# Optimization experiments

Hardware: AMD Instinct MI355X
Metric: run time of the kernel (lower is better)

The kernel has to match this reference:

```python
import jax, jax.numpy as jnp
import numpy as np

NEG_INF = -1e9  # finite large-negative for the additive causal mask
N, H, S, SKV, K, V = 4, 16, 2048, 2048, 128, 128


def setup_inputs() -> dict:
    key = jax.random.key(0)
    k1, k2, k3, k4 = jax.random.split(key, 4)
    seqs = jax.random.normal(k1, (N, H, S, K), dtype=jnp.float32)
    keys = jax.random.normal(k2, (N, H, SKV, K), dtype=jnp.float32)
    values = jax.random.normal(k3, (N, H, SKV, V), dtype=jnp.float32)
    # boolean keep-mask; force first key position valid so no row is fully masked
    kpm = jax.random.randint(k4, (N, SKV), 0, 2) > 0
    kpm = kpm.at[:, 0].set(True)
    # causal additive attention mask, shape (S, S_kv)
    causal = jnp.tril(jnp.ones((S, SKV), dtype=bool))
    attn_mask = jnp.where(causal, 0.0, NEG_INF).astype(jnp.float32)
    return {"seqs": seqs, "keys": keys, "values": values,
            "key_padding_mask": kpm, "attn_mask": attn_mask}


def reference(seqs, keys, values, key_padding_mask, attn_mask):
    # attn_weights: [N,H,S,S_kv]
    scale = seqs.shape[-1] ** -0.5
    w = jnp.einsum('bhsk,bhtk->bhst', seqs, keys) * scale
    w = w + attn_mask  # broadcast (S,S_kv) over (N,H)
    w = jnp.where(key_padding_mask[:, None, None, :], w, -jnp.inf)
    # softmax computed in fp32, then cast back to input dtype (matches torch)
    p = jax.nn.softmax(w.astype(jnp.float32), axis=-1).astype(seqs.dtype)
    attn = jnp.einsum('bhst,bhtv->bhsv', p, values)
    return attn
```

## Files before the change

### kernel.cpp

```cpp
#include <hip/hip_runtime.h>

#define N_B 4
#define N_H 16
#define S_Q 2048
#define S_KV 2048
#define D_K 128
#define NH (N_B * N_H)
#define SCALE 0.08838834764831845f
#define NEG_INF (-__builtin_inff())

typedef __attribute__((ext_vector_type(8))) short s16x8;
typedef __attribute__((ext_vector_type(16))) float f32x16;

__device__ __attribute__((aligned(16))) unsigned short g_Kb[(size_t)NH * S_KV * D_K];
__device__ __attribute__((aligned(16))) unsigned short g_Vt[(size_t)NH * D_K * S_KV];

__device__ inline unsigned short f2bf(float f) {
  unsigned int u = __float_as_uint(f);
  u += 0x7FFFu + ((u >> 16) & 1u);
  return (unsigned short)(u >> 16);
}

__global__ __launch_bounds__(256) void prep_k_kernel(const float* __restrict__ K) {
  size_t g = (size_t)blockIdx.x * 256 + threadIdx.x;
  const float* src = K + g * 8;
  float4 x = *(const float4*)src;
  float4 y = *(const float4*)(src + 4);
  union { uint4 q; unsigned short u[8]; } t;
  t.u[0] = f2bf(x.x); t.u[1] = f2bf(x.y); t.u[2] = f2bf(x.z); t.u[3] = f2bf(x.w);
  t.u[4] = f2bf(y.x); t.u[5] = f2bf(y.y); t.u[6] = f2bf(y.z); t.u[7] = f2bf(y.w);
  ((uint4*)g_Kb)[g] = t.q;
}

__global__ __launch_bounds__(256) void prep_v_kernel(const float* __restrict__ V) {
  __shared__ float tile[32][33];
  int bid = blockIdx.x;
  int bh = bid >> 8;
  int rem = bid & 255;
  int t0 = (rem >> 2) << 5;
  int v0 = (rem & 3) << 5;
  int c = threadIdx.x & 31;
  int r0 = threadIdx.x >> 5;
#pragma unroll
  for (int i = 0; i < 4; i++) {
    int r = r0 + i * 8;
    tile[r][c] = V[((size_t)bh * S_KV + t0 + r) * D_K + v0 + c];
  }
  __syncthreads();
#pragma unroll
  for (int i = 0; i < 4; i++) {
    int r = r0 + i * 8;
    g_Vt[((size_t)bh * D_K + v0 + r) * S_KV + t0 + c] = f2bf(tile[c][r]);
  }
}

__global__ __launch_bounds__(256, 2) void attn_kernel(const float* __restrict__ Q,
                                                      const int* __restrict__ kpm,
                                                      float* __restrict__ out) {
  __shared__ unsigned short sK[32 * 136];
  __shared__ unsigned short sV[128 * 40];
  __shared__ unsigned short sP[4 * 32 * 40];
  __shared__ float sM[32];

  const int bx = blockIdx.x;
  const int bh = ((bx & 7) << 3) | ((bx >> 3) & 7);
  const int q0 = (bx >> 6) << 7;
  const int tid = threadIdx.x;
  const int w = tid >> 6;
  const int ln = tid & 31;
  const int half = (tid >> 5) & 1;
  const int qw = q0 + w * 32;
  const int b = bh >> 4;

  s16x8 qf[8];
  {
    const float* qrow = Q + ((size_t)(bh * S_Q + qw + ln)) * D_K + half * 8;
#pragma unroll
    for (int kc = 0; kc < 8; kc++) {
      float4 x = *(const float4*)(qrow + kc * 16);
      float4 y = *(const float4*)(qrow + kc * 16 + 4);
      union { s16x8 v; unsigned short u[8]; } t;
      t.u[0] = f2bf(x.x * SCALE); t.u[1] = f2bf(x.y * SCALE);
      t.u[2] = f2bf(x.z * SCALE); t.u[3] = f2bf(x.w * SCALE);
      t.u[4] = f2bf(y.x * SCALE); t.u[5] = f2bf(y.y * SCALE);
      t.u[6] = f2bf(y.z * SCALE); t.u[7] = f2bf(y.w * SCALE);
      qf[kc] = t.v;
    }
  }
  s16x8 ones;
  {
    union { s16x8 v; unsigned short u[8]; } t;
#pragma unroll
    for (int j = 0; j < 8; j++) t.u[j] = 0x3F80;
    ones = t.v;
  }

  f32x16 o[4] = {f32x16{}, f32x16{}, f32x16{}, f32x16{}};
  f32x16 sl = {};

  const int kv_end = q0 + 128;
  for (int t0 = 0; t0 < kv_end; t0 += 32) {
    __syncthreads();
#pragma unroll
    for (int p = 0; p < 2; p++) {
      int id = p * 256 + tid;
      int r = id >> 4, cc = id & 15;
      *(uint4*)&sK[r * 136 + cc * 8] =
          *(const uint4*)&g_Kb[((size_t)(bh * S_KV + t0 + r)) * D_K + cc * 8];
      int rv = id >> 2, cv = id & 3;
      *(uint4*)&sV[rv * 40 + cv * 8] =
          *(const uint4*)&g_Vt[((size_t)(bh * D_K + rv)) * S_KV + t0 + cv * 8];
    }
    if (tid < 32) sM[tid] = kpm[b * S_KV + t0 + tid] ? 0.0f : NEG_INF;
    __syncthreads();
    if (t0 > qw + 31) continue;

    const float kf = sM[ln];
    f32x16 sa = {};
#pragma unroll
    for (int kc = 0; kc < 8; kc++) {
      s16x8 kb = *(const s16x8*)&sK[ln * 136 + kc * 16 + half * 8];
      sa = __builtin_amdgcn_mfma_f32_32x32x16_bf16(qf[kc], kb, sa, 0, 0, 0);
    }
    const int tg = t0 + ln;
    unsigned short* pb = &sP[w * 1280];
#pragma unroll
    for (int r = 0; r < 16; r++) {
      int row_l = (r & 3) + ((r >> 2) << 3) + (half << 2);
      float sv = sa[r] + kf;
      sv = (tg <= qw + row_l) ? sv : NEG_INF;
      pb[row_l * 40 + ln] = f2bf(__expf(sv));
    }
    __asm__ __volatile__("s_waitcnt lgkmcnt(0)" ::: "memory");
    s16x8 pa0 = *(const s16x8*)&pb[ln * 40 + half * 8];
    s16x8 pa1 = *(const s16x8*)&pb[ln * 40 + 16 + half * 8];
#pragma unroll
    for (int vt = 0; vt < 4; vt++) {
      s16x8 v0 = *(const s16x8*)&sV[(vt * 32 + ln) * 40 + half * 8];
      s16x8 v1 = *(const s16x8*)&sV[(vt * 32 + ln) * 40 + 16 + half * 8];
      o[vt] = __builtin_amdgcn_mfma_f32_32x32x16_bf16(pa0, v0, o[vt], 0, 0, 0);
      o[vt] = __builtin_amdgcn_mfma_f32_32x32x16_bf16(pa1, v1, o[vt], 0, 0, 0);
    }
    sl = __builtin_amdgcn_mfma_f32_32x32x16_bf16(pa0, ones, sl, 0, 0, 0);
    sl = __builtin_amdgcn_mfma_f32_32x32x16_bf16(pa1, ones, sl, 0, 0, 0);
  }

#pragma unroll
  for (int r = 0; r < 16; r++) {
    int row_l = (r & 3) + ((r >> 2) << 3) + (half << 2);
    float invl = 1.0f / sl[r];
    size_t ob = ((size_t)(bh * S_Q + qw + row_l)) * D_K + ln;
    out[ob]      = o[0][r] * invl;
    out[ob + 32] = o[1][r] * invl;
    out[ob + 64] = o[2][r] * invl;
    out[ob + 96] = o[3][r] * invl;
  }
}

extern "C" void kernel_launch(void* const* d_in, const int* in_sizes, int n_in,
                              void* d_out, int out_size, void* d_ws, size_t ws_size,
                              hipStream_t stream) {
  const float* Q = (const float*)d_in[0];
  const float* K = (const float*)d_in[1];
  const float* V = (const float*)d_in[2];
  const int* kpm = (const int*)d_in[3];
  float* out = (float*)d_out;
  hipLaunchKernelGGL(prep_k_kernel, dim3(8192), dim3(256), 0, stream, K);
  hipLaunchKernelGGL(prep_v_kernel, dim3(16384), dim3(256), 0, stream, V);
  hipLaunchKernelGGL(attn_kernel, dim3(1024), dim3(256), 0, stream, Q, kpm, out);
}
```

Measured before the change: 360.3 us.

## Rework attention kernel: double-buffered tiles, register P transpose, bitmask masking, balanced scheduling

Rewrites the attention kernel. K/V tiles are double-buffered with a register prefetch, so there is one barrier per tile instead of two. The score MFMA is transposed so P stays in registers via permlane32_swap instead of going through shared memory. Key-padding and causal masks become ballot-built bitmasks, exp is replaced by exp2 with log2e folded into the Q scale, and the row sum is taken in VALU rather than with extra MFMAs. Query-tile order is remapped to balance causal work across blocks, output stores become vectorized float4, and the V transpose prep is reworked to emit 16-byte bf16 stores. The risks are added register pressure and that the permlane builtin or asm must be available.

```diff
diff --git a/kernel.cpp b/kernel.cpp
--- a/kernel.cpp
+++ b/kernel.cpp
@@ -1,13 +1,10 @@
 #include <hip/hip_runtime.h>
 
-#define N_B 4
-#define N_H 16
 #define S_Q 2048
 #define S_KV 2048
 #define D_K 128
-#define NH (N_B * N_H)
-#define SCALE 0.08838834764831845f
-#define NEG_INF (-__builtin_inff())
+#define NH 64
+#define QSCALE 0.12751494907890272f
 
 typedef __attribute__((ext_vector_type(8))) short s16x8;
 typedef __attribute__((ext_vector_type(16))) float f32x16;
@@ -19,6 +16,16 @@
   unsigned int u = __float_as_uint(f);
   u += 0x7FFFu + ((u >> 16) & 1u);
   return (unsigned short)(u >> 16);
+}
+
+__device__ inline void plane32_swap(unsigned& a, unsigned& b) {
+#if __has_builtin(__builtin_amdgcn_permlane32_swap)
+  typedef unsigned __attribute__((ext_vector_type(2))) u32x2;
+  u32x2 r = __builtin_amdgcn_permlane32_swap(a, b, false, false);
+  a = r.x; b = r.y;
+#else
+  asm volatile("v_permlane32_swap_b32 %0, %1" : "+v"(a), "+v"(b));
+#endif
 }
 
 __global__ __launch_bounds__(256) void prep_k_kernel(const float* __restrict__ K) {
@@ -33,127 +40,171 @@
 }
 
 __global__ __launch_bounds__(256) void prep_v_kernel(const float* __restrict__ V) {
-  __shared__ float tile[32][33];
+  __shared__ float tile_f[64][33];
   int bid = blockIdx.x;
-  int bh = bid >> 8;
-  int rem = bid & 255;
-  int t0 = (rem >> 2) << 5;
+  int bh = bid >> 7;
+  int rem = bid & 127;
+  int t0 = (rem >> 2) << 6;
   int v0 = (rem & 3) << 5;
   int c = threadIdx.x & 31;
-  int r0 = threadIdx.x >> 5;
-#pragma unroll
-  for (int i = 0; i < 4; i++) {
-    int r = r0 + i * 8;
-    tile[r][c] = V[((size_t)bh * S_KV + t0 + r) * D_K + v0 + c];
+  int r8 = threadIdx.x >> 5;
+#pragma unroll
+  for (int i = 0; i < 8; i++) {
+    int r = r8 + i * 8;
+    tile_f[r][c] = V[((size_t)(bh * S_KV + t0 + r)) * D_K + v0 + c];
   }
   __syncthreads();
-#pragma unroll
-  for (int i = 0; i < 4; i++) {
-    int r = r0 + i * 8;
-    g_Vt[((size_t)bh * D_K + v0 + r) * S_KV + t0 + c] = f2bf(tile[c][r]);
-  }
+  int vv = threadIdx.x >> 3;
+  int jc = threadIdx.x & 7;
+  union { uint4 q; unsigned short u[8]; } t;
+#pragma unroll
+  for (int u8 = 0; u8 < 8; u8++) t.u[u8] = f2bf(tile_f[jc * 8 + u8][vv]);
+  *(uint4*)&g_Vt[((size_t)(bh * D_K + v0 + vv)) * S_KV + t0 + jc * 8] = t.q;
 }
 
 __global__ __launch_bounds__(256, 2) void attn_kernel(const float* __restrict__ Q,
                                                       const int* __restrict__ kpm,
                                                       float* __restrict__ out) {
-  __shared__ unsigned short sK[32 * 136];
-  __shared__ unsigned short sV[128 * 40];
-  __shared__ unsigned short sP[4 * 32 * 40];
-  __shared__ float sM[32];
+  __shared__ unsigned short sK[2][32 * 136];
+  __shared__ unsigned short sV[2][128 * 40];
+  __shared__ unsigned sMask[64];
 
   const int bx = blockIdx.x;
   const int bh = ((bx & 7) << 3) | ((bx >> 3) & 7);
-  const int q0 = (bx >> 6) << 7;
+  int qp = bx >> 6;
+  int qi = (qp & 4) ? ((qp & 8) ? qp - 8 : qp - 4) : ((qp & 8) ? 19 - qp : 15 - qp);
+  const int q0 = qi << 7;
   const int tid = threadIdx.x;
   const int w = tid >> 6;
   const int ln = tid & 31;
-  const int half = (tid >> 5) & 1;
+  const int h = (tid >> 5) & 1;
+  const int h8 = h * 8;
   const int qw = q0 + w * 32;
+  const int qln = qw + ln;
   const int b = bh >> 4;
+
+  {
+    int base = w * 512;
+#pragma unroll
+    for (int rr = 0; rr < 8; rr++) {
+      int idx = base + rr * 64 + (tid & 63);
+      unsigned long long bal = __ballot(kpm[b * S_KV + idx] != 0);
+      if ((tid & 63) == 0) {
+        sMask[(base >> 5) + rr * 2] = (unsigned)bal;
+        sMask[(base >> 5) + rr * 2 + 1] = (unsigned)(bal >> 32);
+      }
+    }
+  }
 
   s16x8 qf[8];
   {
-    const float* qrow = Q + ((size_t)(bh * S_Q + qw + ln)) * D_K + half * 8;
+    const float* qrow = Q + ((size_t)(bh * S_Q + qln)) * D_K + h8;
 #pragma unroll
     for (int kc = 0; kc < 8; kc++) {
       float4 x = *(const float4*)(qrow + kc * 16);
       float4 y = *(const float4*)(qrow + kc * 16 + 4);
       union { s16x8 v; unsigned short u[8]; } t;
-      t.u[0] = f2bf(x.x * SCALE); t.u[1] = f2bf(x.y * SCALE);
-      t.u[2] = f2bf(x.z * SCALE); t.u[3] = f2bf(x.w * SCALE);
-      t.u[4] = f2bf(y.x * SCALE); t.u[5] = f2bf(y.y * SCALE);
-      t.u[6] = f2bf(y.z * SCALE); t.u[7] = f2bf(y.w * SCALE);
+      t.u[0] = f2bf(x.x * QSCALE); t.u[1] = f2bf(x.y * QSCALE);
+      t.u[2] = f2bf(x.z * QSCALE); t.u[3] = f2bf(x.w * QSCALE);
+      t.u[4] = f2bf(y.x * QSCALE); t.u[5] = f2bf(y.y * QSCALE);
+      t.u[6] = f2bf(y.z * QSCALE); t.u[7] = f2bf(y.w * QSCALE);
       qf[kc] = t.v;
     }
   }
-  s16x8 ones;
-  {
-    union { s16x8 v; unsigned short u[8]; } t;
-#pragma unroll
-    for (int j = 0; j < 8; j++) t.u[j] = 0x3F80;
-    ones = t.v;
-  }
+
+  const int id0 = tid, id1 = 256 + tid;
+  const int kr0r = id0 >> 4, kr0c = (id0 & 15) * 8;
+  const int kr1r = id1 >> 4, kr1c = (id1 & 15) * 8;
+  const int vr0r = id0 >> 2, vr0c = (id0 & 3) * 8;
+  const int vr1r = id1 >> 2, vr1c = (id1 & 3) * 8;
+  uint4 rk0, rk1, rv0, rv1;
+  auto load_tile = [&](int t0) {
+    rk0 = *(const uint4*)&g_Kb[((size_t)(bh * S_KV + t0 + kr0r)) * D_K + kr0c];
+    rk1 = *(const uint4*)&g_Kb[((size_t)(bh * S_KV + t0 + kr1r)) * D_K + kr1c];
+    rv0 = *(const uint4*)&g_Vt[((size_t)(bh * D_K + vr0r)) * S_KV + t0 + vr0c];
+    rv1 = *(const uint4*)&g_Vt[((size_t)(bh * D_K + vr1r)) * S_KV + t0 + vr1c];
+  };
+  auto store_tile = [&](int buf) {
+    *(uint4*)&sK[buf][kr0r * 136 + kr0c] = rk0;
+    *(uint4*)&sK[buf][kr1r * 136 + kr1c] = rk1;
+    *(uint4*)&sV[buf][vr0r * 40 + vr0c] = rv0;
+    *(uint4*)&sV[buf][vr1r * 40 + vr1c] = rv1;
+  };
 
   f32x16 o[4] = {f32x16{}, f32x16{}, f32x16{}, f32x16{}};
-  f32x16 sl = {};
-
-  const int kv_end = q0 + 128;
-  for (int t0 = 0; t0 < kv_end; t0 += 32) {
+  float lsum = 0.0f;
+
+  const int nT = qi * 4 + 4;
+  load_tile(0);
+  store_tile(0);
+  load_tile(32);
+  __syncthreads();
+
+  for (int i = 0; i < nT; i++) {
+    const int cur = i & 1;
+    if (i + 1 < nT) {
+      store_tile(1 - cur);
+      if (i + 2 < nT) load_tile((i + 2) * 32);
+    }
+    const int t0 = i * 32;
+    if (t0 <= qw + 31) {
+      const unsigned km = sMask[i];
+      f32x16 sa = {};
+#pragma unroll
+      for (int kc = 0; kc < 8; kc++) {
+        s16x8 kb = *(const s16x8*)&sK[cur][ln * 136 + kc * 16 + h8];
+        sa = __builtin_amdgcn_mfma_f32_32x32x16_bf16(kb, qf[kc], sa, 0, 0, 0);
+      }
+      int thr = qln - t0;
+      unsigned causal = (thr >= 31) ? 0xFFFFFFFFu : ((thr < 0) ? 0u : ((2u << thr) - 1u));
+      unsigned pmh = (km & causal) >> (h * 4);
+      float p[16];
+#pragma unroll
+      for (int r = 0; r < 16; r++) {
+        const int tb = (r & 3) + 8 * (r >> 2);
+        float e = __builtin_amdgcn_exp2f(sa[r]);
+        float bitf = (float)((pmh >> tb) & 1u);
+        p[r] = e * bitf;
+        lsum += p[r];
+      }
+      unsigned d[8];
+#pragma unroll
+      for (int m = 0; m < 4; m++) {
+        d[2 * m] = __builtin_amdgcn_perm(__float_as_uint(p[4 * m + 1]),
+                                         __float_as_uint(p[4 * m + 0]), 0x07060302u);
+        d[2 * m + 1] = __builtin_amdgcn_perm(__float_as_uint(p[4 * m + 3]),
+                                             __float_as_uint(p[4 * m + 2]), 0x07060302u);
+      }
+      plane32_swap(d[0], d[2]); plane32_swap(d[1], d[3]);
+      plane32_swap(d[4], d[6]); plane32_swap(d[5], d[7]);
+      union { unsigned u[4]; s16x8 v; } pu0, pu1;
+      pu0.u[0] = d[0]; pu0.u[1] = d[1]; pu0.u[2] = d[2]; pu0.u[3] = d[3];
+      pu1.u[0] = d[4]; pu1.u[1] = d[5]; pu1.u[2] = d[6]; pu1.u[3] = d[7];
+#pragma unroll
+      for (int vt = 0; vt < 4; vt++) {
+        s16x8 va = *(const s16x8*)&sV[cur][(vt * 32 + ln) * 40 + h8];
+        s16x8 vb = *(const s16x8*)&sV[cur][(vt * 32 + ln) * 40 + 16 + h8];
+        o[vt] = __builtin_amdgcn_mfma_f32_32x32x16_bf16(va, pu0.v, o[vt], 0, 0, 0);
+        o[vt] = __builtin_amdgcn_mfma_f32_32x32x16_bf16(vb, pu1.v, o[vt], 0, 0, 0);
+      }
+    }
     __syncthreads();
-#pragma unroll
-    for (int p = 0; p < 2; p++) {
-      int id = p * 256 + tid;
-      int r = id >> 4, cc = id & 15;
-      *(uint4*)&sK[r * 136 + cc * 8] =
-          *(const uint4*)&g_Kb[((size_t)(bh * S_KV + t0 + r)) * D_K + cc * 8];
-      int rv = id >> 2, cv = id & 3;
-      *(uint4*)&sV[rv * 40 + cv * 8] =
-          *(const uint4*)&g_Vt[((size_t)(bh * D_K + rv)) * S_KV + t0 + cv * 8];
-    }
-    if (tid < 32) sM[tid] = kpm[b * S_KV + t0 + tid] ? 0.0f : NEG_INF;
-    __syncthreads();
-    if (t0 > qw + 31) continue;
-
-    const float kf = sM[ln];
-    f32x16 sa = {};
-#pragma unroll
-    for (int kc = 0; kc < 8; kc++) {
-      s16x8 kb = *(const s16x8*)&sK[ln * 136 + kc * 16 + half * 8];
-      sa = __builtin_amdgcn_mfma_f32_32x32x16_bf16(qf[kc], kb, sa, 0, 0, 0);
-    }
-    const int tg = t0 + ln;
-    unsigned short* pb = &sP[w * 1280];
-#pragma unroll
-    for (int r = 0; r < 16; r++) {
-      int row_l = (r & 3) + ((r >> 2) << 3) + (half << 2);
-      float sv = sa[r] + kf;
-      sv = (tg <= qw + row_l) ? sv : NEG_INF;
-      pb[row_l * 40 + ln] = f2bf(__expf(sv));
-    }
-    __asm__ __volatile__("s_waitcnt lgkmcnt(0)" ::: "memory");
-    s16x8 pa0 = *(const s16x8*)&pb[ln * 40 + half * 8];
-    s16x8 pa1 = *(const s16x8*)&pb[ln * 40 + 16 + half * 8];
-#pragma unroll
-    for (int vt = 0; vt < 4; vt++) {
-      s16x8 v0 = *(const s16x8*)&sV[(vt * 32 + ln) * 40 + half * 8];
-      s16x8 v1 = *(const s16x8*)&sV[(vt * 32 + ln) * 40 + 16 + half * 8];
-      o[vt] = __builtin_amdgcn_mfma_f32_32x32x16_bf16(pa0, v0, o[vt], 0, 0, 0);
-      o[vt] = __builtin_amdgcn_mfma_f32_32x32x16_bf16(pa1, v1, o[vt], 0, 0, 0);
-    }
-    sl = __builtin_amdgcn_mfma_f32_32x32x16_bf16(pa0, ones, sl, 0, 0, 0);
-    sl = __builtin_amdgcn_mfma_f32_32x32x16_bf16(pa1, ones, sl, 0, 0, 0);
-  }
-
-#pragma unroll
-  for (int r = 0; r < 16; r++) {
-    int row_l = (r & 3) + ((r >> 2) << 3) + (half << 2);
-    float invl = 1.0f / sl[r];
-    size_t ob = ((size_t)(bh * S_Q + qw + row_l)) * D_K + ln;
-    out[ob]      = o[0][r] * invl;
-    out[ob + 32] = o[1][r] * invl;
-    out[ob + 64] = o[2][r] * invl;
-    out[ob + 96] = o[3][r] * invl;
+  }
+
+  float ltot = lsum + __shfl_xor(lsum, 32, 64);
+  float invl = 1.0f / ltot;
+  size_t orow = ((size_t)(bh * S_Q + qln)) * D_K;
+#pragma unroll
+  for (int vt = 0; vt < 4; vt++) {
+#pragma unroll
+    for (int qd = 0; qd < 4; qd++) {
+      float4 vv;
+      vv.x = o[vt][4 * qd + 0] * invl;
+      vv.y = o[vt][4 * qd + 1] * invl;
+      vv.z = o[vt][4 * qd + 2] * invl;
+      vv.w = o[vt][4 * qd + 3] * invl;
+      *(float4*)&out[orow + vt * 32 + qd * 8 + 4 * h] = vv;
+    }
   }
 }
 
@@ -166,6 +217,6 @@
   const int* kpm = (const int*)d_in[3];
   float* out = (float*)d_out;
   hipLaunchKernelGGL(prep_k_kernel, dim3(8192), dim3(256), 0, stream, K);
-  hipLaunchKernelGGL(prep_v_kernel, dim3(16384), dim3(256), 0, stream, V);
+  hipLaunchKernelGGL(prep_v_kernel, dim3(8192), dim3(256), 0, stream, V);
   hipLaunchKernelGGL(attn_kernel, dim3(1024), dim3(256), 0, stream, Q, kpm, out);
 }
```

New measurement: 323.4 us. -10.2%, faster.
